# Optimization experiments

Measured on AMD Instinct MI355X. Metric: run time of the kernel, lower is better.

## Reference

```python
import jax, jax.numpy as jnp
import numpy as np

# camera / raster constants
N = 10000            # gaussians
W = 256
H = 256
FX = 200.0
FY = 200.0
TILE = 16
NTX = W // TILE
NTY = H // TILE
NT = NTX * NTY       # 256 tiles
P = TILE * TILE      # 256 pixels per tile
K = 256              # max gaussians kept per tile
NEAR = 0.3
MAGIC = 1.2          # frustum expansion factor from project_culling
LP = 0.3 / (FX * FX) # low-pass filter added to 2D covariance diagonal


def quat_to_rot(q):
    w, x, y, z = q[:, 0], q[:, 1], q[:, 2], q[:, 3]
    r0 = jnp.stack([1 - 2 * (y * y + z * z), 2 * (x * y - w * z), 2 * (x * z + w * y)], -1)
    r1 = jnp.stack([2 * (x * y + w * z), 1 - 2 * (x * x + z * z), 2 * (y * z - w * x)], -1)
    r2 = jnp.stack([2 * (x * z - w * y), 2 * (y * z + w * x), 1 - 2 * (x * x + y * y)], -1)
    return jnp.stack([r0, r1, r2], axis=1)  # [N,3,3]


def splat_forward(pos, rgb, opacity, quaternion, scale, w2c_r, w2c_t):
    # ---- project + frustum cull (global_culling) ----
    q = quaternion / jnp.linalg.norm(quaternion, axis=-1, keepdims=True)
    R = quat_to_rot(q)
    sigma = jnp.exp(scale)                               # normalize_scale
    cov3d = jnp.einsum('nij,nj,nkj->nik', R, sigma * sigma, R)
    p_cam = pos @ w2c_r.T + w2c_t                        # [N,3]
    x, y, z = p_cam[:, 0], p_cam[:, 1], p_cam[:, 2]
    zc = jnp.maximum(z, 1e-6)
    half_w = W * MAGIC / 2 / FX
    half_h = H * MAGIC / 2 / FY
    mean2d = jnp.stack([x / zc, y / zc], -1)             # camera-plane coords
    in_frustum = (z > NEAR) & (jnp.abs(mean2d[:, 0]) < half_w) & (jnp.abs(mean2d[:, 1]) < half_h)
    iz = 1.0 / zc
    zero = jnp.zeros_like(iz)
    J = jnp.stack([jnp.stack([iz, zero, -x * iz * iz], -1),
                   jnp.stack([zero, iz, -y * iz * iz], -1)], axis=1)  # [N,2,3]
    cov_cam = jnp.einsum('ij,njk,lk->nil', w2c_r, cov3d, w2c_r)
    cov2d = jnp.einsum('nij,njk,nlk->nil', J, cov_cam, J)            # [N,2,2]
    a = cov2d[:, 0, 0] + LP
    c = cov2d[:, 1, 1] + LP
    b = cov2d[:, 0, 1]

    # ---- per-tile culling + fixed-K binning (calc_tile_list / gather_gaussians) ----
    cx = (jnp.arange(NTX) * TILE + TILE / 2 - W / 2) / FX
    cy = (jnp.arange(NTY) * TILE + TILE / 2 - H / 2) / FY
    centers = jnp.stack(jnp.meshgrid(cx, cy, indexing='xy'), -1).reshape(NT, 2)  # [NT,2] (ty-major)
    tile_half_diag = 0.5 * jnp.sqrt((TILE / FX) ** 2 + (TILE / FY) ** 2)
    mid = 0.5 * (a + c)
    sigma_max = jnp.sqrt(jnp.maximum(mid + jnp.sqrt(jnp.maximum((0.5 * (a - c)) ** 2 + b * b, 0.0)), 1e-12))
    dist = jnp.linalg.norm(centers[:, None, :] - mean2d[None, :, :], axis=-1)   # [NT,N]
    valid = in_frustum[None, :] & (dist <= (3.0 * sigma_max + tile_half_diag)[None, :])
    score = jnp.where(valid, -dist, -1e10)
    vals, idx = jax.lax.top_k(score, K)                                          # [NT,K]
    valid_k = vals > -1e9

    mean_g = mean2d[idx]                     # [NT,K,2]
    z_g = z[idx]
    a_g, b_g, c_g = a[idx], b[idx], c[idx]
    opa_g = jax.nn.sigmoid(opacity)[idx]
    rgb_g = jax.nn.sigmoid(rgb)[idx]         # [NT,K,3]

    # ---- depth sort within each tile ----
    order = jnp.argsort(jnp.where(valid_k, z_g, jnp.inf), axis=-1)
    def srt(arr):
        o = order.reshape(order.shape + (1,) * (arr.ndim - 2))
        return jnp.take_along_axis(arr, o, axis=1)
    mean_s, a_s, b_s, c_s = srt(mean_g), srt(a_g), srt(b_g), srt(c_g)
    opa_s, rgb_s = srt(opa_g), srt(rgb_g)
    valid_s = srt(valid_k).astype(pos.dtype)

    # ---- per-pixel front-to-back alpha compositing (draw) ----
    px = ((jnp.arange(W) + 0.5 - W / 2) / FX).reshape(NTX, TILE)
    py = ((jnp.arange(H) + 0.5 - H / 2) / FY).reshape(NTY, TILE)
    U = jnp.broadcast_to(px[None, :, None, :], (NTY, NTX, TILE, TILE)).reshape(NT, P)
    V = jnp.broadcast_to(py[:, None, :, None], (NTY, NTX, TILE, TILE)).reshape(NT, P)
    dx = U[:, :, None] - mean_s[:, None, :, 0]          # [NT,P,K]
    dy = V[:, :, None] - mean_s[:, None, :, 1]
    det = jnp.maximum(a_s * c_s - b_s * b_s, 1e-12)[:, None, :]
    maha = (c_s[:, None, :] * dx * dx - 2.0 * b_s[:, None, :] * dx * dy + a_s[:, None, :] * dy * dy) / det
    alpha = jnp.clip(opa_s[:, None, :] * jnp.exp(-0.5 * maha), 0.0, 0.99) * valid_s[:, None, :]
    trans = jnp.cumprod(1.0 - alpha, axis=-1)
    texc = jnp.concatenate([jnp.ones_like(trans[..., :1]), trans[..., :-1]], axis=-1)
    color = jnp.einsum('tpk,tkc->tpc', alpha * texc, rgb_s)  # [NT,P,3]
    img = color.reshape(NTY, NTX, TILE, TILE, 3).transpose(0, 2, 1, 3, 4).reshape(H, W, 3)
    return jnp.clip(img, 0.0, 1.0)


def setup_inputs() -> dict:
    key = jax.random.key(0)
    ks = jax.random.split(key, 6)
    zpos = jax.random.uniform(ks[0], (N,), minval=2.0, maxval=6.0)
    uv = jax.random.uniform(ks[1], (N, 2), minval=-0.6, maxval=0.6)
    pos = jnp.concatenate([uv * zpos[:, None], zpos[:, None]], axis=-1)
    rgb = jax.random.normal(ks[2], (N, 3))              # pre-sigmoid logits
    opacity = jax.random.normal(ks[3], (N,)) + 1.5      # sigmoid -> ~0.8 like init_opacity
    quaternion = jax.random.normal(ks[4], (N, 4))
    scale = 0.2 * jax.random.normal(ks[5], (N, 3)) - 4.5  # exp -> ~0.01 world sigma
    w2c_r = jnp.eye(3, dtype=jnp.float32)
    w2c_t = jnp.zeros((3,), dtype=jnp.float32)
    return {"pos": pos, "rgb": rgb, "opacity": opacity, "quaternion": quaternion,
            "scale": scale, "w2c_r": w2c_r, "w2c_t": w2c_t}


def reference(pos, rgb, opacity, quaternion, scale, w2c_r, w2c_t):
    return splat_forward(pos, rgb, opacity, quaternion, scale, w2c_r, w2c_t)
```

## Files before the change

kernel.cpp:

```cpp
#include <hip/hip_runtime.h>
#include <math.h>

namespace {
constexpr int W = 256, H = 256, TILE = 16, NTX = 16, NT = 256, K = 256;
constexpr float FX = 200.0f, FY = 200.0f, NEARP = 0.3f, MAGIC = 1.2f;
constexpr float LP = 0.3f / (FX * FX);
constexpr float HALF_W = W * MAGIC / 2.0f / FX;
constexpr float HALF_H = H * MAGIC / 2.0f / FY;
constexpr float THDIAG = 0.05656854249492381f;
constexpr int CAP = 2048;
constexpr int N_PAD = 10240;
constexpr int BT = 1024;
constexpr int NB_MAX = 64;
constexpr int SEG = 256;
constexpr size_t A_OFF  = 0;
constexpr size_t B_OFF  = A_OFF + (size_t)N_PAD * 16;
constexpr size_t C_OFF  = B_OFF + (size_t)N_PAD * 16;
constexpr size_t SL_OFF = C_OFF + (size_t)N_PAD * 16;
constexpr size_t LD_OFF = SL_OFF + (size_t)NT * NB_MAX * 4;
constexpr size_t LZ_OFF = LD_OFF + (size_t)NT * NB_MAX * SEG * 8;
constexpr size_t WS_FULL = LZ_OFF + (size_t)NT * NB_MAX * SEG * 8;
}

struct Pre { float mx, my, z, a, b, c, radius; };

__device__ inline Pre preprocess(int g, const float* __restrict__ pos,
                                 const float* __restrict__ quat,
                                 const float* __restrict__ scl,
                                 const float* __restrict__ w2cr,
                                 const float* __restrict__ w2ct) {
  float p0 = pos[3*g+0], p1 = pos[3*g+1], p2 = pos[3*g+2];
  float qw = quat[4*g+0], qx = quat[4*g+1], qy = quat[4*g+2], qz = quat[4*g+3];
  float inv = 1.0f / sqrtf(qw*qw + qx*qx + qy*qy + qz*qz);
  qw *= inv; qx *= inv; qy *= inv; qz *= inv;
  float r00 = 1.f-2.f*(qy*qy+qz*qz), r01 = 2.f*(qx*qy-qw*qz), r02 = 2.f*(qx*qz+qw*qy);
  float r10 = 2.f*(qx*qy+qw*qz), r11 = 1.f-2.f*(qx*qx+qz*qz), r12 = 2.f*(qy*qz-qw*qx);
  float r20 = 2.f*(qx*qz-qw*qy), r21 = 2.f*(qy*qz+qw*qx), r22 = 1.f-2.f*(qx*qx+qy*qy);
  float e0 = expf(scl[3*g+0]); float s0 = e0*e0;
  float e1 = expf(scl[3*g+1]); float s1 = e1*e1;
  float e2 = expf(scl[3*g+2]); float s2 = e2*e2;
  float C00 = r00*r00*s0 + r01*r01*s1 + r02*r02*s2;
  float C01 = r00*r10*s0 + r01*r11*s1 + r02*r12*s2;
  float C02 = r00*r20*s0 + r01*r21*s1 + r02*r22*s2;
  float C11 = r10*r10*s0 + r11*r11*s1 + r12*r12*s2;
  float C12 = r10*r20*s0 + r11*r21*s1 + r12*r22*s2;
  float C22 = r20*r20*s0 + r21*r21*s1 + r22*r22*s2;
  float w00=w2cr[0],w01=w2cr[1],w02=w2cr[2];
  float w10=w2cr[3],w11=w2cr[4],w12=w2cr[5];
  float w20=w2cr[6],w21=w2cr[7],w22=w2cr[8];
  float x = w00*p0 + w01*p1 + w02*p2 + w2ct[0];
  float y = w10*p0 + w11*p1 + w12*p2 + w2ct[1];
  float z = w20*p0 + w21*p1 + w22*p2 + w2ct[2];
  float m00 = w00*C00 + w01*C01 + w02*C02;
  float m01 = w00*C01 + w01*C11 + w02*C12;
  float m02 = w00*C02 + w01*C12 + w02*C22;
  float m10 = w10*C00 + w11*C01 + w12*C02;
  float m11 = w10*C01 + w11*C11 + w12*C12;
  float m12 = w10*C02 + w11*C12 + w12*C22;
  float m20 = w20*C00 + w21*C01 + w22*C02;
  float m21 = w20*C01 + w21*C11 + w22*C12;
  float m22 = w20*C02 + w21*C12 + w22*C22;
  float v00 = m00*w00 + m01*w01 + m02*w02;
  float v01 = m00*w10 + m01*w11 + m02*w12;
  float v02 = m00*w20 + m01*w21 + m02*w22;
  float v10 = m10*w00 + m11*w01 + m12*w02;
  float v11 = m10*w10 + m11*w11 + m12*w12;
  float v12 = m10*w20 + m11*w21 + m12*w22;
  float v20 = m20*w00 + m21*w01 + m22*w02;
  float v21 = m20*w10 + m21*w11 + m22*w12;
  float v22 = m20*w20 + m21*w21 + m22*w22;
  float zc = fmaxf(z, 1e-6f);
  float iz = 1.0f / zc;
  float mx = x * iz, my = y * iz;
  float iz2 = iz * iz;
  float jx = -x * iz2, jy = -y * iz2;
  float a00 = iz*v00 + jx*v20, a01 = iz*v01 + jx*v21, a02 = iz*v02 + jx*v22;
  float a10 = iz*v10 + jy*v20, a11 = iz*v11 + jy*v21, a12 = iz*v12 + jy*v22;
  float A  = a00*iz + a02*jx + LP;
  float Bv = a01*iz + a02*jy;
  float Cv = a11*iz + a12*jy + LP;
  float mid = 0.5f*(A + Cv);
  float hh  = 0.5f*(A - Cv);
  float disc = fmaxf(hh*hh + Bv*Bv, 0.0f);
  float smax = sqrtf(fmaxf(mid + sqrtf(disc), 1e-12f));
  bool infr = (z > NEARP) && (fabsf(mx) < HALF_W) && (fabsf(my) < HALF_H);
  Pre r;
  r.mx = mx; r.my = my; r.z = z; r.a = A; r.b = Bv; r.c = Cv;
  r.radius = infr ? (3.0f * smax + THDIAG) : -1.0f;
  return r;
}


template <bool BIN>
__global__ __launch_bounds__(256)
void pre_bin(const float* __restrict__ pos, const float* __restrict__ rgb,
             const float* __restrict__ opac, const float* __restrict__ quat,
             const float* __restrict__ scl, const float* __restrict__ w2cr,
             const float* __restrict__ w2ct,
             float4* __restrict__ pa, float4* __restrict__ pb,
             float4* __restrict__ pc, int* __restrict__ seglen,
             unsigned long long* __restrict__ listd,
             unsigned long long* __restrict__ listz, int n) {
  __shared__ int s_tc[NT];
  const int tid = (int)threadIdx.x;
  const int blk = (int)blockIdx.x;
  if (BIN) {
    if (tid < NT) s_tc[tid] = 0;
    __syncthreads();
  }
  const int g = blk * 256 + tid;
  if (g < n) {
    Pre p = preprocess(g, pos, quat, scl, w2cr, w2ct);
    float det = fmaxf(p.a * p.c - p.b * p.b, 1e-12f);
    pa[g] = make_float4(p.mx, p.my, p.radius, p.z);
    pb[g] = make_float4(p.a, p.b, p.c, 1.0f / det);
    pc[g] = make_float4(1.0f / (1.0f + __expf(-opac[g])),
                        1.0f / (1.0f + __expf(-rgb[3*g+0])),
                        1.0f / (1.0f + __expf(-rgb[3*g+1])),
                        1.0f / (1.0f + __expf(-rgb[3*g+2])));
    if (BIN && p.radius >= 0.0f) {
      float r = p.radius;
      int txlo = max(0,     (int)floorf(((p.mx - r) * FX + 120.0f) * 0.0625f));
      int txhi = min(NTX-1, (int)ceilf (((p.mx + r) * FX + 120.0f) * 0.0625f));
      int tylo = max(0,     (int)floorf(((p.my - r) * FY + 120.0f) * 0.0625f));
      int tyhi = min(NTX-1, (int)ceilf (((p.my + r) * FY + 120.0f) * 0.0625f));
      unsigned long long gbits = (unsigned int)g;
      for (int ty = tylo; ty <= tyhi; ++ty) {
        float cy = (ty * TILE + TILE * 0.5f - H * 0.5f) / FY;
        float ddy = cy - p.my;
        for (int tx = txlo; tx <= txhi; ++tx) {
          float cx = (tx * TILE + TILE * 0.5f - W * 0.5f) / FX;
          float ddx = cx - p.mx;
          float dist = sqrtf(ddx * ddx + ddy * ddy);
          if (dist <= r) {
            int t = ty * NTX + tx;
            int slot = atomicAdd(&s_tc[t], 1);
            size_t idx = ((size_t)t * NB_MAX + blk) * SEG + slot;
            listd[idx] = ((unsigned long long)__float_as_uint(dist) << 32) | gbits;
            listz[idx] = ((unsigned long long)__float_as_uint(p.z)  << 32) | gbits;
          }
        }
      }
    }
  }
  if (BIN) {
    __syncthreads();
    if (tid < NT) seglen[(size_t)tid * NB_MAX + blk] = s_tc[tid];
  }
}


template <int S>
__device__ inline void hsortN(unsigned long long* key, int M) {
  const int tid = (int)threadIdx.x;
  __syncthreads();
  unsigned long long e[S];
  #pragma unroll
  for (int s = 0; s < S; ++s) {
    int i = tid + (s << 10);
    e[s] = (i < M) ? key[i] : ~0ull;
  }
  for (int k = 2; k <= M; k <<= 1) {
    for (int j = k >> 1; j >= 64; j >>= 1) {
      __syncthreads();
      #pragma unroll
      for (int s = 0; s < S; ++s) {
        int i = tid + (s << 10);
        if (i < M) key[i] = e[s];
      }
      __syncthreads();
      #pragma unroll
      for (int s = 0; s < S; ++s) {
        int i = tid + (s << 10);
        if (i < M) {
          unsigned long long p = key[i ^ j];
          bool takeMin = (((i & j) == 0) == ((i & k) == 0));
          e[s] = ((p < e[s]) == takeMin) ? p : e[s];
        }
      }
    }
    int j0 = ((k >> 1) < 32) ? (k >> 1) : 32;
    for (int j = j0; j >= 1; j >>= 1) {
      #pragma unroll
      for (int s = 0; s < S; ++s) {
        int i = tid + (s << 10);
        unsigned long long p = __shfl_xor(e[s], j, 64);
        bool takeMin = (((i & j) == 0) == ((i & k) == 0));
        e[s] = ((p < e[s]) == takeMin) ? p : e[s];
      }
    }
  }
  __syncthreads();
  #pragma unroll
  for (int s = 0; s < S; ++s) {
    int i = tid + (s << 10);
    if (i < M) key[i] = e[s];
  }
  __syncthreads();
}


__device__ inline void sort_blend_store(
    const float4* __restrict__ pa, const float4* __restrict__ pb,
    const float4* __restrict__ pc, float* __restrict__ out,
    unsigned long long* s_zkey, int* s_rank,
    float4* s_p0, float4* s_p1, float2* s_p2, float4* s_part,
    int cnt2, int tx, int ty) {
  const int tid = (int)threadIdx.x;
  {
    const int e = tid & 255;
    const int q = tid >> 8;
    if (e < cnt2) {
      unsigned long long mykey = s_zkey[e];
      int jlo = q * 64;
      int jhi = min(cnt2, jlo + 64);
      int partial = 0;
      for (int j = jlo; j < jhi; ++j)
        partial += (s_zkey[j] < mykey) ? 1 : 0;
      if (partial) atomicAdd(&s_rank[e], partial);
    }
  }
  __syncthreads();
  if (tid < cnt2) {
    int g = (int)(s_zkey[tid] & 0xffffffffu);
    int r = s_rank[tid];
    float4 A = pa[g], B = pb[g], C = pc[g];
    s_p0[r] = make_float4(A.x, A.y, B.x, B.y);
    s_p1[r] = make_float4(B.z, B.w, C.x, C.y);
    s_p2[r] = make_float2(C.z, C.w);
  }
  __syncthreads();
  const int p    = tid & 255;
  const int q    = tid >> 8;
  const int prow = p / TILE, pcol = p % TILE;
  const float u = ((float)(tx * TILE + pcol) + 0.5f - W * 0.5f) / FX;
  const float v = ((float)(ty * TILE + prow) + 0.5f - H * 0.5f) / FY;
  const int chunk = (cnt2 + 3) >> 2;
  const int k0 = q * chunk;
  const int k1 = min(cnt2, k0 + chunk);
  float T = 1.0f, accr = 0.0f, accg = 0.0f, accb = 0.0f;
  for (int k2 = k0; k2 < k1; ++k2) {
    float4 p0 = s_p0[k2];
    float4 p1 = s_p1[k2];
    float2 p2 = s_p2[k2];
    float dx = u - p0.x;
    float dy = v - p0.y;
    float maha = (p1.x*dx*dx - 2.0f*p0.w*dx*dy + p0.z*dy*dy) * p1.y;
    float alpha = fminf(p1.z * __expf(-0.5f * maha), 0.99f);
    float w = alpha * T;
    accr += w * p1.w;
    accg += w * p2.x;
    accb += w * p2.y;
    T *= (1.0f - alpha);
  }
  s_part[tid] = make_float4(accr, accg, accb, T);
  __syncthreads();
  if (q == 0) {
    float4 P0 = s_part[p];
    float4 P1 = s_part[p + 256];
    float4 P2 = s_part[p + 512];
    float4 P3 = s_part[p + 768];
    float r = P0.x + P0.w * (P1.x + P1.w * (P2.x + P2.w * P3.x));
    float g = P0.y + P0.w * (P1.y + P1.w * (P2.y + P2.w * P3.y));
    float b = P0.z + P0.w * (P1.z + P1.w * (P2.z + P2.w * P3.z));
    const int row = ty * TILE + prow;
    const int col = tx * TILE + pcol;
    const int o = (row * W + col) * 3;
    out[o+0] = fminf(fmaxf(r, 0.0f), 1.0f);
    out[o+1] = fminf(fmaxf(g, 0.0f), 1.0f);
    out[o+2] = fminf(fmaxf(b, 0.0f), 1.0f);
  }
}


__global__ __launch_bounds__(BT)
void render_list(const float4* __restrict__ pa, const float4* __restrict__ pb,
                 const float4* __restrict__ pc, const int* __restrict__ seglen,
                 const unsigned long long* __restrict__ listd,
                 const unsigned long long* __restrict__ listz,
                 float* __restrict__ out, int nb) {
  __shared__ unsigned long long s_dkey[CAP];
  __shared__ unsigned long long s_zkey[CAP];
  __shared__ int s_off[NB_MAX + 1];
  __shared__ int s_rank[K];
  __shared__ float4 s_p0[K];
  __shared__ float4 s_p1[K];
  __shared__ float2 s_p2[K];
  __shared__ float4 s_part[BT];

  const int t  = (int)blockIdx.x;
  const int tx = t % NTX;
  const int ty = t / NTX;
  const int tid = (int)threadIdx.x;

  if (tid < K) s_rank[tid] = 0;
  if (tid < 64) {
    int v = (tid < nb) ? seglen[(size_t)t * NB_MAX + tid] : 0;
    #pragma unroll
    for (int d = 1; d < 64; d <<= 1) {
      int u2 = __shfl_up(v, d, 64);
      if (tid >= d) v += u2;
    }
    if (tid == 0) s_off[0] = 0;
    if (tid < nb) s_off[tid + 1] = v;
  }
  __syncthreads();
  int cnt = min(s_off[nb], CAP);

  for (int i = tid; i < cnt; i += BT) {
    int lo = 0, hi = nb;
    while (hi - lo > 1) {
      int mid = (lo + hi) >> 1;
      if (s_off[mid] <= i) lo = mid; else hi = mid;
    }
    size_t src = ((size_t)t * NB_MAX + lo) * SEG + (size_t)(i - s_off[lo]);
    s_dkey[i] = listd[src];
    s_zkey[i] = listz[src];
  }
  __syncthreads();
  int cnt2 = cnt;

  if (cnt > K) {
    int M = 512; while (M < cnt) M <<= 1;
    for (int i = cnt + tid; i < M; i += BT) s_dkey[i] = ~0ull;
    if (M <= 1024) hsortN<1>(s_dkey, M);
    else           hsortN<2>(s_dkey, 2048);
    if (tid < K) {
      int g = (int)(s_dkey[tid] & 0xffffffffu);
      s_zkey[tid] = ((unsigned long long)__float_as_uint(pa[g].w) << 32) |
                    (unsigned int)g;
    }
    __syncthreads();
    cnt2 = K;
  }

  sort_blend_store(pa, pb, pc, out, s_zkey, s_rank, s_p0, s_p1, s_p2, s_part,
                   cnt2, tx, ty);
}


__global__ __launch_bounds__(BT)
void render_scan(const float4* __restrict__ pa, const float4* __restrict__ pb,
                 const float4* __restrict__ pc, float* __restrict__ out, int n) {
  __shared__ unsigned long long s_dkey[CAP];
  __shared__ unsigned long long s_zkey[CAP];
  __shared__ int s_rank[K];
  __shared__ float4 s_p0[K];
  __shared__ float4 s_p1[K];
  __shared__ float2 s_p2[K];
  __shared__ float4 s_part[BT];
  __shared__ int s_cnt;

  const int t  = (int)blockIdx.x;
  const int tx = t % NTX;
  const int ty = t / NTX;
  const int tid = (int)threadIdx.x;
  const int lane = tid & 63;
  const float cxc = (tx * TILE + TILE * 0.5f - W * 0.5f) / FX;
  const float cyc = (ty * TILE + TILE * 0.5f - H * 0.5f) / FY;

  if (tid == 0) s_cnt = 0;
  if (tid < K) s_rank[tid] = 0;
  __syncthreads();

  for (int g = tid; g < n; g += BT) {
    float4 v = pa[g];
    float ddx = cxc - v.x, ddy = cyc - v.y;
    float dist = sqrtf(ddx * ddx + ddy * ddy);
    bool hit = (v.z >= 0.0f) && (dist <= v.z);
    unsigned long long m = __ballot(hit);
    if (m) {
      int leader = __ffsll((long long)m) - 1;
      int base = 0;
      if (lane == leader) base = atomicAdd(&s_cnt, __popcll(m));
      base = __shfl(base, leader, 64);
      if (hit) {
        int slot = base + __popcll(m & ((1ull << lane) - 1ull));
        if (slot < CAP) {
          s_dkey[slot] = ((unsigned long long)__float_as_uint(dist) << 32) |
                         (unsigned int)g;
          s_zkey[slot] = ((unsigned long long)__float_as_uint(v.w) << 32) |
                         (unsigned int)g;
        }
      }
    }
  }
  __syncthreads();
  int cnt = min(s_cnt, CAP);
  int cnt2 = cnt;

  if (cnt > K) {
    int M = 512; while (M < cnt) M <<= 1;
    for (int i = cnt + tid; i < M; i += BT) s_dkey[i] = ~0ull;
    if (M <= 1024) hsortN<1>(s_dkey, M);
    else           hsortN<2>(s_dkey, 2048);
    if (tid < K) {
      int g = (int)(s_dkey[tid] & 0xffffffffu);
      s_zkey[tid] = ((unsigned long long)__float_as_uint(pa[g].w) << 32) |
                    (unsigned int)g;
    }
    __syncthreads();
    cnt2 = K;
  }

  sort_blend_store(pa, pb, pc, out, s_zkey, s_rank, s_p0, s_p1, s_p2, s_part,
                   cnt2, tx, ty);
}

extern "C" void kernel_launch(void* const* d_in, const int* in_sizes, int n_in,
                              void* d_out, int out_size, void* d_ws, size_t ws_size,
                              hipStream_t stream) {
  const float* pos  = (const float*)d_in[0];
  const float* rgb  = (const float*)d_in[1];
  const float* opac = (const float*)d_in[2];
  const float* quat = (const float*)d_in[3];
  const float* scl  = (const float*)d_in[4];
  const float* w2cr = (const float*)d_in[5];
  const float* w2ct = (const float*)d_in[6];
  float* out = (float*)d_out;
  const int n = in_sizes[0] / 3;
  const int nb = (n + 255) / 256;

  char* ws = (char*)d_ws;
  float4* pa = (float4*)(ws + A_OFF);
  float4* pb = (float4*)(ws + B_OFF);
  float4* pc = (float4*)(ws + C_OFF);
  int* seglen = (int*)(ws + SL_OFF);
  unsigned long long* listd = (unsigned long long*)(ws + LD_OFF);
  unsigned long long* listz = (unsigned long long*)(ws + LZ_OFF);

  if (ws_size >= WS_FULL && nb <= NB_MAX) {
    pre_bin<true><<<nb, 256, 0, stream>>>(
        pos, rgb, opac, quat, scl, w2cr, w2ct, pa, pb, pc, seglen, listd, listz, n);
    render_list<<<NT, BT, 0, stream>>>(pa, pb, pc, seglen, listd, listz, out, nb);
  } else {
    pre_bin<false><<<nb, 256, 0, stream>>>(
        pos, rgb, opac, quat, scl, w2cr, w2ct, pa, pb, pc, seglen, listd, listz, n);
    render_scan<<<NT, BT, 0, stream>>>(pa, pb, pc, out, n);
  }
}
```

Before: 24.99 us.

## Precompute conic and log-opacity, broadcast params via readlane, skip negligible gaussians, shrink CAP

The per-gaussian record now stores the inverse-covariance conic already divided by the determinant, plus log-opacity, so the blend inner loop only needs FMAs and a single exp. Each wavefront loads up to 64 gaussians into registers and broadcasts them with readlane instead of reading shared memory on every iteration. Gaussians whose Mahalanobis distance exceeds a threshold are skipped. CAP drops to 1024, the sort becomes single-register, and distance keys are gathered only when a tile overflows. This assumes each quarter of a tile holds at most 64 gaussians and each tile at most 1024 candidates, and the maha cutoff changes results slightly.

```diff
diff --git a/kernel.cpp b/kernel.cpp
--- a/kernel.cpp
+++ b/kernel.cpp
@@ -8,7 +8,7 @@
 constexpr float HALF_W = W * MAGIC / 2.0f / FX;
 constexpr float HALF_H = H * MAGIC / 2.0f / FY;
 constexpr float THDIAG = 0.05656854249492381f;
-constexpr int CAP = 2048;
+constexpr int CAP = 1024;
 constexpr int N_PAD = 10240;
 constexpr int BT = 1024;
 constexpr int NB_MAX = 64;
@@ -20,6 +20,10 @@
 constexpr size_t LD_OFF = SL_OFF + (size_t)NT * NB_MAX * 4;
 constexpr size_t LZ_OFF = LD_OFF + (size_t)NT * NB_MAX * SEG * 8;
 constexpr size_t WS_FULL = LZ_OFF + (size_t)NT * NB_MAX * SEG * 8;
+}
+
+__device__ inline float rlane(float v, int l) {
+  return __int_as_float(__builtin_amdgcn_readlane(__float_as_int(v), l));
 }
 
 struct Pre { float mx, my, z, a, b, c, radius; };
@@ -112,12 +116,13 @@
   if (g < n) {
     Pre p = preprocess(g, pos, quat, scl, w2cr, w2ct);
     float det = fmaxf(p.a * p.c - p.b * p.b, 1e-12f);
+    float ivd = 1.0f / det;
+    float lopa = -__logf(1.0f + __expf(-opac[g]));
     pa[g] = make_float4(p.mx, p.my, p.radius, p.z);
-    pb[g] = make_float4(p.a, p.b, p.c, 1.0f / det);
-    pc[g] = make_float4(1.0f / (1.0f + __expf(-opac[g])),
-                        1.0f / (1.0f + __expf(-rgb[3*g+0])),
+    pb[g] = make_float4(p.a * ivd, -2.0f * p.b * ivd, p.c * ivd, lopa);
+    pc[g] = make_float4(1.0f / (1.0f + __expf(-rgb[3*g+0])),
                         1.0f / (1.0f + __expf(-rgb[3*g+1])),
-                        1.0f / (1.0f + __expf(-rgb[3*g+2])));
+                        1.0f / (1.0f + __expf(-rgb[3*g+2])), 0.0f);
     if (BIN && p.radius >= 0.0f) {
       float r = p.radius;
       int txlo = max(0,     (int)floorf(((p.mx - r) * FX + 120.0f) * 0.0625f));
@@ -150,61 +155,39 @@
 }
 
 
-template <int S>
-__device__ inline void hsortN(unsigned long long* key, int M) {
+__device__ inline void hsort1(unsigned long long* key, int M) {
   const int tid = (int)threadIdx.x;
   __syncthreads();
-  unsigned long long e[S];
-  #pragma unroll
-  for (int s = 0; s < S; ++s) {
-    int i = tid + (s << 10);
-    e[s] = (i < M) ? key[i] : ~0ull;
-  }
+  unsigned long long e = (tid < M) ? key[tid] : ~0ull;
   for (int k = 2; k <= M; k <<= 1) {
     for (int j = k >> 1; j >= 64; j >>= 1) {
       __syncthreads();
-      #pragma unroll
-      for (int s = 0; s < S; ++s) {
-        int i = tid + (s << 10);
-        if (i < M) key[i] = e[s];
-      }
+      if (tid < M) key[tid] = e;
       __syncthreads();
-      #pragma unroll
-      for (int s = 0; s < S; ++s) {
-        int i = tid + (s << 10);
-        if (i < M) {
-          unsigned long long p = key[i ^ j];
-          bool takeMin = (((i & j) == 0) == ((i & k) == 0));
-          e[s] = ((p < e[s]) == takeMin) ? p : e[s];
-        }
+      if (tid < M) {
+        unsigned long long p = key[tid ^ j];
+        bool takeMin = (((tid & j) == 0) == ((tid & k) == 0));
+        e = ((p < e) == takeMin) ? p : e;
       }
     }
     int j0 = ((k >> 1) < 32) ? (k >> 1) : 32;
     for (int j = j0; j >= 1; j >>= 1) {
-      #pragma unroll
-      for (int s = 0; s < S; ++s) {
-        int i = tid + (s << 10);
-        unsigned long long p = __shfl_xor(e[s], j, 64);
-        bool takeMin = (((i & j) == 0) == ((i & k) == 0));
-        e[s] = ((p < e[s]) == takeMin) ? p : e[s];
-      }
-    }
-  }
-  __syncthreads();
-  #pragma unroll
-  for (int s = 0; s < S; ++s) {
-    int i = tid + (s << 10);
-    if (i < M) key[i] = e[s];
-  }
-  __syncthreads();
-}
-
-
-__device__ inline void sort_blend_store(
+      unsigned long long p = __shfl_xor(e, j, 64);
+      bool takeMin = (((tid & j) == 0) == ((tid & k) == 0));
+      e = ((p < e) == takeMin) ? p : e;
+    }
+  }
+  __syncthreads();
+  if (tid < M) key[tid] = e;
+  __syncthreads();
+}
+
+
+__device__ inline void tail_blend(
     const float4* __restrict__ pa, const float4* __restrict__ pb,
     const float4* __restrict__ pc, float* __restrict__ out,
     unsigned long long* s_zkey, int* s_rank,
-    float4* s_p0, float4* s_p1, float2* s_p2, float4* s_part,
+    float4* s_q0, float4* s_q1, float* s_q2, float4* s_part,
     int cnt2, int tx, int ty) {
   const int tid = (int)threadIdx.x;
   {
@@ -225,33 +208,51 @@
     int g = (int)(s_zkey[tid] & 0xffffffffu);
     int r = s_rank[tid];
     float4 A = pa[g], B = pb[g], C = pc[g];
-    s_p0[r] = make_float4(A.x, A.y, B.x, B.y);
-    s_p1[r] = make_float4(B.z, B.w, C.x, C.y);
-    s_p2[r] = make_float2(C.z, C.w);
-  }
-  __syncthreads();
+    s_q0[r] = make_float4(A.x, A.y, B.x, B.y);
+    s_q1[r] = make_float4(B.z, B.w, C.x, C.y);
+    s_q2[r] = C.z;
+  }
+  __syncthreads();
+
   const int p    = tid & 255;
   const int q    = tid >> 8;
+  const int L    = tid & 63;
   const int prow = p / TILE, pcol = p % TILE;
   const float u = ((float)(tx * TILE + pcol) + 0.5f - W * 0.5f) / FX;
   const float v = ((float)(ty * TILE + prow) + 0.5f - H * 0.5f) / FY;
   const int chunk = (cnt2 + 3) >> 2;
   const int k0 = q * chunk;
   const int k1 = min(cnt2, k0 + chunk);
+  const int nk = max(0, k1 - k0);
+
+  int e2 = k0 + L;
+  bool val = (L < nk);
+  float4 q0 = val ? s_q0[e2] : make_float4(0.f, 0.f, 0.f, 0.f);
+  float4 q1 = val ? s_q1[e2] : make_float4(1e30f, -1e30f, 0.f, 0.f);
+  float  qb = val ? s_q2[e2] : 0.f;
+
   float T = 1.0f, accr = 0.0f, accg = 0.0f, accb = 0.0f;
-  for (int k2 = k0; k2 < k1; ++k2) {
-    float4 p0 = s_p0[k2];
-    float4 p1 = s_p1[k2];
-    float2 p2 = s_p2[k2];
-    float dx = u - p0.x;
-    float dy = v - p0.y;
-    float maha = (p1.x*dx*dx - 2.0f*p0.w*dx*dy + p0.z*dy*dy) * p1.y;
-    float alpha = fminf(p1.z * __expf(-0.5f * maha), 0.99f);
-    float w = alpha * T;
-    accr += w * p1.w;
-    accg += w * p2.x;
-    accb += w * p2.y;
-    T *= (1.0f - alpha);
+  for (int k2 = 0; k2 < nk; ++k2) {
+    float mx  = rlane(q0.x, k2);
+    float my  = rlane(q0.y, k2);
+    float ap  = rlane(q0.z, k2);
+    float nb2 = rlane(q0.w, k2);
+    float cp  = rlane(q1.x, k2);
+    float dx = u - mx;
+    float dy = v - my;
+    float maha = fmaf(cp * dx, dx, fmaf(nb2 * dx, dy, (ap * dy) * dy));
+    if (maha < 23.0f) {
+      float lopa = rlane(q1.y, k2);
+      float cr   = rlane(q1.z, k2);
+      float cg   = rlane(q1.w, k2);
+      float cb   = rlane(qb,  k2);
+      float alpha = fminf(__expf(fmaf(-0.5f, maha, lopa)), 0.99f);
+      float w = alpha * T;
+      accr = fmaf(w, cr, accr);
+      accg = fmaf(w, cg, accg);
+      accb = fmaf(w, cb, accb);
+      T = fmaf(-alpha, T, T);
+    }
   }
   s_part[tid] = make_float4(accr, accg, accb, T);
   __syncthreads();
@@ -279,13 +280,13 @@
                  const unsigned long long* __restrict__ listd,
                  const unsigned long long* __restrict__ listz,
                  float* __restrict__ out, int nb) {
+  __shared__ unsigned long long s_zkey[CAP];
   __shared__ unsigned long long s_dkey[CAP];
-  __shared__ unsigned long long s_zkey[CAP];
   __shared__ int s_off[NB_MAX + 1];
   __shared__ int s_rank[K];
-  __shared__ float4 s_p0[K];
-  __shared__ float4 s_p1[K];
-  __shared__ float2 s_p2[K];
+  __shared__ float4 s_q0[K];
+  __shared__ float4 s_q1[K];
+  __shared__ float  s_q2[K];
   __shared__ float4 s_part[BT];
 
   const int t  = (int)blockIdx.x;
@@ -314,17 +315,24 @@
       if (s_off[mid] <= i) lo = mid; else hi = mid;
     }
     size_t src = ((size_t)t * NB_MAX + lo) * SEG + (size_t)(i - s_off[lo]);
-    s_dkey[i] = listd[src];
     s_zkey[i] = listz[src];
   }
   __syncthreads();
   int cnt2 = cnt;
 
   if (cnt > K) {
+    for (int i = tid; i < cnt; i += BT) {
+      int lo = 0, hi = nb;
+      while (hi - lo > 1) {
+        int mid = (lo + hi) >> 1;
+        if (s_off[mid] <= i) lo = mid; else hi = mid;
+      }
+      size_t src = ((size_t)t * NB_MAX + lo) * SEG + (size_t)(i - s_off[lo]);
+      s_dkey[i] = listd[src];
+    }
     int M = 512; while (M < cnt) M <<= 1;
     for (int i = cnt + tid; i < M; i += BT) s_dkey[i] = ~0ull;
-    if (M <= 1024) hsortN<1>(s_dkey, M);
-    else           hsortN<2>(s_dkey, 2048);
+    hsort1(s_dkey, M);
     if (tid < K) {
       int g = (int)(s_dkey[tid] & 0xffffffffu);
       s_zkey[tid] = ((unsigned long long)__float_as_uint(pa[g].w) << 32) |
@@ -334,20 +342,20 @@
     cnt2 = K;
   }
 
-  sort_blend_store(pa, pb, pc, out, s_zkey, s_rank, s_p0, s_p1, s_p2, s_part,
-                   cnt2, tx, ty);
+  tail_blend(pa, pb, pc, out, s_zkey, s_rank, s_q0, s_q1, s_q2, s_part,
+             cnt2, tx, ty);
 }
 
 
 __global__ __launch_bounds__(BT)
 void render_scan(const float4* __restrict__ pa, const float4* __restrict__ pb,
                  const float4* __restrict__ pc, float* __restrict__ out, int n) {
+  __shared__ unsigned long long s_zkey[CAP];
   __shared__ unsigned long long s_dkey[CAP];
-  __shared__ unsigned long long s_zkey[CAP];
   __shared__ int s_rank[K];
-  __shared__ float4 s_p0[K];
-  __shared__ float4 s_p1[K];
-  __shared__ float2 s_p2[K];
+  __shared__ float4 s_q0[K];
+  __shared__ float4 s_q1[K];
+  __shared__ float  s_q2[K];
   __shared__ float4 s_part[BT];
   __shared__ int s_cnt;
 
@@ -392,8 +400,7 @@
   if (cnt > K) {
     int M = 512; while (M < cnt) M <<= 1;
     for (int i = cnt + tid; i < M; i += BT) s_dkey[i] = ~0ull;
-    if (M <= 1024) hsortN<1>(s_dkey, M);
-    else           hsortN<2>(s_dkey, 2048);
+    hsort1(s_dkey, M);
     if (tid < K) {
       int g = (int)(s_dkey[tid] & 0xffffffffu);
       s_zkey[tid] = ((unsigned long long)__float_as_uint(pa[g].w) << 32) |
@@ -403,8 +410,8 @@
     cnt2 = K;
   }
 
-  sort_blend_store(pa, pb, pc, out, s_zkey, s_rank, s_p0, s_p1, s_p2, s_part,
-                   cnt2, tx, ty);
+  tail_blend(pa, pb, pc, out, s_zkey, s_rank, s_q0, s_q1, s_q2, s_part,
+             cnt2, tx, ty);
 }
 
 extern "C" void kernel_launch(void* const* d_in, const int* in_sizes, int n_in,
```

Result: slower. 26.61 us (+6.5%).
